# Optimization experiments

Measured on AMD Instinct MI355X. Metric: run time of the kernel, lower is better.

Reference implementation:

```python
import jax, jax.numpy as jnp
import numpy as np

TEMPERATURE = 0.5

def setup_inputs() -> dict:
    key = jax.random.key(0)
    k1, k2 = jax.random.split(key)
    B, D = 4096, 256
    return {
        "first_transformed": jax.random.normal(k1, (B, D), dtype=jnp.float32),
        "second_transformed": jax.random.normal(k2, (B, D), dtype=jnp.float32),
    }

def reference(first_transformed, second_transformed):
    B = first_transformed.shape[0]
    z = jnp.concatenate([first_transformed, second_transformed], axis=0)  # [2B, D]
    z = z / jnp.linalg.norm(z, axis=1, keepdims=True)
    sim = jnp.matmul(z, z.T) / TEMPERATURE  # [2B, 2B]
    n = 2 * B
    # exclude self-similarity from the denominator (mask diagonal)
    diag_mask = jnp.eye(n, dtype=bool)
    denom = jax.nn.logsumexp(jnp.where(diag_mask, -jnp.inf, sim), axis=1)  # [2B]
    # positive pair for row i is row (i+B) mod 2B
    pos_idx = (jnp.arange(n) + B) % n
    pos = sim[jnp.arange(n), pos_idx]  # [2B]
    # loss = 1/(2B) * sum_i (-log(exp(pos_i)/denom_i)) = mean(denom - pos)
    return jnp.mean(denom - pos)
```

## Files before the change

kernel.cpp:

```cpp
#include <hip/hip_runtime.h>
#include <hip/hip_bf16.h>
#include <math.h>


#define NROWS 8192
#define BHALF 4096
#define DDIM  256
#define ROWB  512
#define JSPLIT 8
#define JCHUNK (NROWS / JSPLIT)
#define JT 64
#define NTILES (JCHUNK / JT)
#define TILEB (JT * ROWB)

#define SQRT_K1 1.6986436f
#define LN2F 0.6931471805599453f

typedef __attribute__((ext_vector_type(8))) __bf16 bf16x8;
typedef __attribute__((ext_vector_type(4))) float f32x4;

#if __has_builtin(__builtin_amdgcn_exp2f)
#define FEXP2(x) __builtin_amdgcn_exp2f(x)
#else
#define FEXP2(x) __exp2f(x)
#endif
#if __has_builtin(__builtin_amdgcn_logf)
#define FLOG2(x) __builtin_amdgcn_logf(x)
#else
#define FLOG2(x) __log2f(x)
#endif

__device__ __forceinline__ float bfu(unsigned short u) {
  union { unsigned v; float f; } x; x.v = ((unsigned)u) << 16; return x.f;
}

__global__ __launch_bounds__(256) void norm_kernel(
    const float* __restrict__ a, const float* __restrict__ b,
    char* __restrict__ zb, float* __restrict__ selfdot) {
  int row = blockIdx.x * 4 + (threadIdx.x >> 6);
  int lane = threadIdx.x & 63;
  const float* src = (row < BHALF) ? (a + (size_t)row * DDIM)
                                   : (b + (size_t)(row - BHALF) * DDIM);
  float4 v = ((const float4*)src)[lane];
  float ss = v.x * v.x + v.y * v.y + v.z * v.z + v.w * v.w;
  #pragma unroll
  for (int m = 1; m < 64; m <<= 1) ss += __shfl_xor(ss, m, 64);
  float inv = rsqrtf(ss);
  inv = inv * (1.5f - 0.5f * ss * inv * inv);
  float sc = inv * SQRT_K1;

  union { __hip_bfloat16 h; unsigned short u; } c0, c1, c2, c3;
  c0.h = __float2bfloat16(v.x * sc);
  c1.h = __float2bfloat16(v.y * sc);
  c2.h = __float2bfloat16(v.z * sc);
  c3.h = __float2bfloat16(v.w * sc);
  float q0 = bfu(c0.u), q1 = bfu(c1.u), q2 = bfu(c2.u), q3 = bfu(c3.u);
  float sq = q0 * q0 + q1 * q1 + q2 * q2 + q3 * q3;
  #pragma unroll
  for (int m = 1; m < 64; m <<= 1) sq += __shfl_xor(sq, m, 64);

  ushort4 o = make_ushort4(c0.u, c1.u, c2.u, c3.u);
  int off = row * ROWB + ((lane * 8) ^ ((row & 7) << 4));
  *(ushort4*)(zb + off) = o;
  if (lane == 0) selfdot[row] = sq;
}

__global__ __launch_bounds__(512, 2) void sim_kernel(
    const char* __restrict__ zb, float* __restrict__ s_part) {
  __shared__ __align__(16) char lds[3 * TILEB];
  int js = blockIdx.x;
  int rb = blockIdx.y;
  int wave = threadIdx.x >> 6;
  int lane = threadIdx.x & 63;
  int lrow = lane & 15;
  int kgrp = lane >> 4;
  int sw = (lrow & 7) << 4;
  int r0 = rb * 256 + wave * 32;
  int jbase = js * JCHUNK;

  int koff[8];
  #pragma unroll
  for (int kk = 0; kk < 8; ++kk) koff[kk] = (kk * 64 + kgrp * 16) ^ sw;

  bf16x8 af[2][8];
  #pragma unroll
  for (int rf = 0; rf < 2; ++rf) {
    const char* rp = zb + (size_t)(r0 + rf * 16 + lrow) * ROWB;
    #pragma unroll
    for (int kk = 0; kk < 8; ++kk)
      af[rf][kk] = *(const bf16x8*)(rp + koff[kk]);
  }

  float sacc[2][4] = {};
  f32x4 X0, X1, Y0, Y1;
  X0 = X1 = Y0 = Y1 = (f32x4){-1e30f, -1e30f, -1e30f, -1e30f};

  #define STAGE1(dstbuf, j0, portion) do {                                    \
    const char* g_ = zb + (size_t)(j0) * ROWB + (portion) * 8192 +            \
                     wave * 1024 + lane * 16;                                 \
    char* l_ = lds + (dstbuf) * TILEB + (portion) * 8192 + wave * 1024;       \
    __builtin_amdgcn_global_load_lds(                                         \
        (const __attribute__((address_space(1))) void*)g_,                    \
        (__attribute__((address_space(3))) void*)l_, 16, 0, 0);               \
  } while (0)

  #define PHASE(ct, C0, C1, P0, P1) do {                                      \
    const char* lbr = lds + buf * TILEB + (ct) * 8192 + lrow * ROWB;          \
    bf16x8 bfv[8];                                                            \
    _Pragma("unroll")                                                         \
    for (int kk = 0; kk < 8; ++kk)                                            \
      bfv[kk] = *(const bf16x8*)(lbr + koff[kk]);                             \
    if (t + 2 < NTILES) STAGE1(dst, jbase + (t + 2) * JT, ct);                \
    _Pragma("unroll")                                                         \
    for (int r = 0; r < 4; ++r) {                                             \
      sacc[0][r] += FEXP2(P0[r]);                                             \
      sacc[1][r] += FEXP2(P1[r]);                                             \
    }                                                                         \
    __builtin_amdgcn_sched_barrier(0);                                        \
    __builtin_amdgcn_s_barrier();                                             \
    C0 = (f32x4){0.f, 0.f, 0.f, 0.f};                                         \
    C1 = (f32x4){0.f, 0.f, 0.f, 0.f};                                         \
    __builtin_amdgcn_s_setprio(1);                                            \
    _Pragma("unroll")                                                         \
    for (int kk = 0; kk < 8; ++kk) {                                          \
      C0 = __builtin_amdgcn_mfma_f32_16x16x32_bf16(af[0][kk], bfv[kk], C0, 0, 0, 0); \
      C1 = __builtin_amdgcn_mfma_f32_16x16x32_bf16(af[1][kk], bfv[kk], C1, 0, 0, 0); \
    }                                                                         \
    __builtin_amdgcn_s_setprio(0);                                            \
    if ((ct) == 3) {                                                          \
      if (t + 2 < NTILES)                                                     \
        asm volatile("s_waitcnt vmcnt(4)" ::: "memory");                      \
      else if (t + 1 < NTILES)                                                \
        asm volatile("s_waitcnt vmcnt(0)" ::: "memory");                      \
      __builtin_amdgcn_sched_barrier(0);                                      \
    }                                                                         \
    __builtin_amdgcn_s_barrier();                                             \
  } while (0)

  #pragma unroll
  for (int p = 0; p < 4; ++p) STAGE1(0, jbase, p);
  #pragma unroll
  for (int p = 0; p < 4; ++p) STAGE1(1, jbase + JT, p);
  asm volatile("s_waitcnt vmcnt(4)" ::: "memory");
  __builtin_amdgcn_sched_barrier(0);
  __builtin_amdgcn_s_barrier();

  int buf = 0;
  for (int t = 0; t < NTILES; ++t) {
    int dst = buf + 2; if (dst >= 3) dst -= 3;
    PHASE(0, X0, X1, Y0, Y1);
    PHASE(1, Y0, Y1, X0, X1);
    PHASE(2, X0, X1, Y0, Y1);
    PHASE(3, Y0, Y1, X0, X1);
    ++buf; if (buf == 3) buf = 0;
  }
  #pragma unroll
  for (int r = 0; r < 4; ++r) {
    sacc[0][r] += FEXP2(Y0[r]);
    sacc[1][r] += FEXP2(Y1[r]);
  }
  #undef PHASE
  #undef STAGE1

  #pragma unroll
  for (int rf = 0; rf < 2; ++rf) {
    #pragma unroll
    for (int r = 0; r < 4; ++r) {
      float v = sacc[rf][r];
      #pragma unroll
      for (int m = 1; m < 16; m <<= 1) v += __shfl_xor(v, m, 64);
      if (lrow == 0) {
        int grow = r0 + rf * 16 + kgrp * 4 + r;
        s_part[(size_t)grow * JSPLIT + js] = v;
      }
    }
  }
}

__global__ __launch_bounds__(256) void rowterm_kernel(
    const char* __restrict__ zb, const float* __restrict__ s_part,
    const float* __restrict__ selfdot, float* __restrict__ bpart) {
  int wave = threadIdx.x >> 6;
  int lane = threadIdx.x & 63;
  int rbase = blockIdx.x * 16 + wave * 4;
  float wacc = 0.f;
  #pragma unroll
  for (int rr = 0; rr < 4; ++rr) {
    int i = rbase + rr;
    int j = i ^ BHALF;
    int wo = (lane * 8) ^ ((i & 7) << 4);
    ushort4 zi = *(const ushort4*)(zb + (size_t)i * ROWB + wo);
    ushort4 zj = *(const ushort4*)(zb + (size_t)j * ROWB + wo);
    float dot = bfu(zi.x) * bfu(zj.x) + bfu(zi.y) * bfu(zj.y) +
                bfu(zi.z) * bfu(zj.z) + bfu(zi.w) * bfu(zj.w);
    float sp = (lane < JSPLIT) ? s_part[(size_t)i * JSPLIT + lane] : 0.f;
    #pragma unroll
    for (int m = 1; m < 64; m <<= 1) {
      dot += __shfl_xor(dot, m, 64);
      sp += __shfl_xor(sp, m, 64);
    }
    float S = sp - FEXP2(selfdot[i]);
    wacc += LN2F * (FLOG2(S) - dot);
  }
  __shared__ float red[4];
  if (lane == 0) red[wave] = wacc;
  __syncthreads();
  if (threadIdx.x == 0)
    bpart[blockIdx.x] = red[0] + red[1] + red[2] + red[3];
}

__global__ __launch_bounds__(512) void final_kernel(
    const float* __restrict__ bpart, float* __restrict__ out) {
  int t = threadIdx.x;
  float v = bpart[t];
  #pragma unroll
  for (int m = 1; m < 64; m <<= 1) v += __shfl_xor(v, m, 64);
  __shared__ float r2[8];
  if ((t & 63) == 0) r2[t >> 6] = v;
  __syncthreads();
  if (t == 0) {
    float s = 0.f;
    #pragma unroll
    for (int w = 0; w < 8; ++w) s += r2[w];
    out[0] = s / (float)NROWS;
  }
}

extern "C" void kernel_launch(void* const* d_in, const int* in_sizes, int n_in,
                              void* d_out, int out_size, void* d_ws, size_t ws_size,
                              hipStream_t stream) {
  const float* a = (const float*)d_in[0];
  const float* b = (const float*)d_in[1];
  float* out = (float*)d_out;
  char* ws = (char*)d_ws;

  char* zb = ws;
  float* selfdot = (float*)(ws + (size_t)NROWS * ROWB);
  float* s_part = selfdot + NROWS;
  float* bpart = s_part + (size_t)NROWS * JSPLIT;

  hipLaunchKernelGGL(norm_kernel, dim3(NROWS / 4), dim3(256), 0, stream,
                     a, b, zb, selfdot);
  hipLaunchKernelGGL(sim_kernel, dim3(JSPLIT, 32), dim3(512), 0, stream,
                     zb, s_part);
  hipLaunchKernelGGL(rowterm_kernel, dim3(512), dim3(256), 0, stream,
                     zb, s_part, selfdot, bpart);
  hipLaunchKernelGGL(final_kernel, dim3(1), dim3(512), 0, stream, bpart, out);
}
```

Measured before the change: 49.96 us.

## Exploit symmetry of similarity matrix by computing only upper-triangle tiles

Replaces the full row-by-column-chunk sweep with a tiled GEMM over 256x128 block pairs that covers only about half of the symmetric similarity matrix, using 1088 blocks. Each tile contributes exp-sums to both its rows and its columns, written into a wider per-row slot array that the rowterm kernel then sums. The inner loop moves from a resident-A, streamed-B scheme to K-sliced double-buffered staging of both operands with large register accumulators. This aims to roughly halve MFMA and exp work, at the cost of extra LDS reductions, more partial slots and higher register pressure.

```diff
diff --git a/kernel.cpp b/kernel.cpp
--- a/kernel.cpp
+++ b/kernel.cpp
@@ -7,11 +7,10 @@
 #define BHALF 4096
 #define DDIM  256
 #define ROWB  512
-#define JSPLIT 8
-#define JCHUNK (NROWS / JSPLIT)
-#define JT 64
-#define NTILES (JCHUNK / JT)
-#define TILEB (JT * ROWB)
+#define NKS   8
+#define BUFB  (24 * 1024)
+#define SSTRIDE 64
+#define NSLOT 49
 
 #define SQRT_K1 1.6986436f
 #define LN2F 0.6931471805599453f
@@ -65,114 +64,128 @@
   if (lane == 0) selfdot[row] = sq;
 }
 
-__global__ __launch_bounds__(512, 2) void sim_kernel(
+__global__ __launch_bounds__(256, 2) void sim_kernel(
     const char* __restrict__ zb, float* __restrict__ s_part) {
-  __shared__ __align__(16) char lds[3 * TILEB];
-  int js = blockIdx.x;
-  int rb = blockIdx.y;
+  __shared__ __align__(16) char lds[2 * BUFB];
+  __shared__ float cred_row[2][256];
+  __shared__ float cred_col[2][128];
+
+  int bid = blockIdx.x;
+  int h = bid & 1;
+  int tg = bid >> 1;
+  int t = tg & 31;
+  int g = tg >> 5;
+  int u = (t + g) & 31;
+  int r0 = t * 256;
+  int c0 = u * 256 + h * 128;
+
   int wave = threadIdx.x >> 6;
+  int wm = wave >> 1, wn = wave & 1;
   int lane = threadIdx.x & 63;
   int lrow = lane & 15;
   int kgrp = lane >> 4;
   int sw = (lrow & 7) << 4;
-  int r0 = rb * 256 + wave * 32;
-  int jbase = js * JCHUNK;
-
-  int koff[8];
-  #pragma unroll
-  for (int kk = 0; kk < 8; ++kk) koff[kk] = (kk * 64 + kgrp * 16) ^ sw;
-
-  bf16x8 af[2][8];
-  #pragma unroll
-  for (int rf = 0; rf < 2; ++rf) {
-    const char* rp = zb + (size_t)(r0 + rf * 16 + lrow) * ROWB;
-    #pragma unroll
-    for (int kk = 0; kk < 8; ++kk)
-      af[rf][kk] = *(const bf16x8*)(rp + koff[kk]);
-  }
-
-  float sacc[2][4] = {};
-  f32x4 X0, X1, Y0, Y1;
-  X0 = X1 = Y0 = Y1 = (f32x4){-1e30f, -1e30f, -1e30f, -1e30f};
-
-  #define STAGE1(dstbuf, j0, portion) do {                                    \
-    const char* g_ = zb + (size_t)(j0) * ROWB + (portion) * 8192 +            \
-                     wave * 1024 + lane * 16;                                 \
-    char* l_ = lds + (dstbuf) * TILEB + (portion) * 8192 + wave * 1024;       \
+
+  f32x4 acc[8][4];
+  #pragma unroll
+  for (int mi = 0; mi < 8; ++mi)
+    #pragma unroll
+    for (int nj = 0; nj < 4; ++nj)
+      acc[mi][nj] = (f32x4){0.f, 0.f, 0.f, 0.f};
+  bf16x8 bfv[4];
+
+  #define STAGE_SLOT(dstbuf, ks, s) do {                                      \
+    int rowb_ = ((s) < 16) ? (r0 + (s) * 16) : (c0 + ((s) - 16) * 16);        \
+    const char* g_ = zb + (size_t)(rowb_ + lrow) * ROWB +                     \
+                     (((ks) * 64 + kgrp * 16) ^ sw);                          \
+    char* l_ = lds + (dstbuf) * BUFB + (s) * 1024;                            \
     __builtin_amdgcn_global_load_lds(                                         \
         (const __attribute__((address_space(1))) void*)g_,                    \
         (__attribute__((address_space(3))) void*)l_, 16, 0, 0);               \
   } while (0)
 
-  #define PHASE(ct, C0, C1, P0, P1) do {                                      \
-    const char* lbr = lds + buf * TILEB + (ct) * 8192 + lrow * ROWB;          \
-    bf16x8 bfv[8];                                                            \
+  #define PHASE(P) do {                                                       \
+    const char* lb_ = lds + buf * BUFB + lane * 16;                           \
+    bf16x8 afv[4];                                                            \
     _Pragma("unroll")                                                         \
-    for (int kk = 0; kk < 8; ++kk)                                            \
-      bfv[kk] = *(const bf16x8*)(lbr + koff[kk]);                             \
-    if (t + 2 < NTILES) STAGE1(dst, jbase + (t + 2) * JT, ct);                \
-    _Pragma("unroll")                                                         \
-    for (int r = 0; r < 4; ++r) {                                             \
-      sacc[0][r] += FEXP2(P0[r]);                                             \
-      sacc[1][r] += FEXP2(P1[r]);                                             \
+    for (int i = 0; i < 4; ++i)                                               \
+      afv[i] = *(const bf16x8*)(lb_ + (wm * 8 + (P) * 4 + i) * 1024);         \
+    if ((P) == 0) {                                                           \
+      _Pragma("unroll")                                                       \
+      for (int nj = 0; nj < 4; ++nj)                                          \
+        bfv[nj] = *(const bf16x8*)(lb_ + (16 + wn * 4 + nj) * 1024);          \
     }                                                                         \
+    if (ks + 1 < NKS) {                                                       \
+      STAGE_SLOT(buf ^ 1, ks + 1, wave + 4 * (3 * (P) + 0));                  \
+      STAGE_SLOT(buf ^ 1, ks + 1, wave + 4 * (3 * (P) + 1));                  \
+      STAGE_SLOT(buf ^ 1, ks + 1, wave + 4 * (3 * (P) + 2));                  \
+    }                                                                         \
+    asm volatile("s_waitcnt lgkmcnt(0)" ::: "memory");                        \
     __builtin_amdgcn_sched_barrier(0);                                        \
     __builtin_amdgcn_s_barrier();                                             \
-    C0 = (f32x4){0.f, 0.f, 0.f, 0.f};                                         \
-    C1 = (f32x4){0.f, 0.f, 0.f, 0.f};                                         \
     __builtin_amdgcn_s_setprio(1);                                            \
     _Pragma("unroll")                                                         \
-    for (int kk = 0; kk < 8; ++kk) {                                          \
-      C0 = __builtin_amdgcn_mfma_f32_16x16x32_bf16(af[0][kk], bfv[kk], C0, 0, 0, 0); \
-      C1 = __builtin_amdgcn_mfma_f32_16x16x32_bf16(af[1][kk], bfv[kk], C1, 0, 0, 0); \
-    }                                                                         \
+    for (int i = 0; i < 4; ++i)                                               \
+      _Pragma("unroll")                                                       \
+      for (int nj = 0; nj < 4; ++nj)                                          \
+        acc[(P) * 4 + i][nj] = __builtin_amdgcn_mfma_f32_16x16x32_bf16(       \
+            afv[i], bfv[nj], acc[(P) * 4 + i][nj], 0, 0, 0);                  \
     __builtin_amdgcn_s_setprio(0);                                            \
-    if ((ct) == 3) {                                                          \
-      if (t + 2 < NTILES)                                                     \
-        asm volatile("s_waitcnt vmcnt(4)" ::: "memory");                      \
-      else if (t + 1 < NTILES)                                                \
-        asm volatile("s_waitcnt vmcnt(0)" ::: "memory");                      \
-      __builtin_amdgcn_sched_barrier(0);                                      \
-    }                                                                         \
+    if ((P) == 1 && ks + 1 < NKS)                                             \
+      asm volatile("s_waitcnt vmcnt(0)" ::: "memory");                        \
+    __builtin_amdgcn_sched_barrier(0);                                        \
     __builtin_amdgcn_s_barrier();                                             \
   } while (0)
 
   #pragma unroll
-  for (int p = 0; p < 4; ++p) STAGE1(0, jbase, p);
-  #pragma unroll
-  for (int p = 0; p < 4; ++p) STAGE1(1, jbase + JT, p);
-  asm volatile("s_waitcnt vmcnt(4)" ::: "memory");
+  for (int i = 0; i < 6; ++i) STAGE_SLOT(0, 0, wave + 4 * i);
+  asm volatile("s_waitcnt vmcnt(0)" ::: "memory");
   __builtin_amdgcn_sched_barrier(0);
   __builtin_amdgcn_s_barrier();
 
-  int buf = 0;
-  for (int t = 0; t < NTILES; ++t) {
-    int dst = buf + 2; if (dst >= 3) dst -= 3;
-    PHASE(0, X0, X1, Y0, Y1);
-    PHASE(1, Y0, Y1, X0, X1);
-    PHASE(2, X0, X1, Y0, Y1);
-    PHASE(3, Y0, Y1, X0, X1);
-    ++buf; if (buf == 3) buf = 0;
-  }
-  #pragma unroll
-  for (int r = 0; r < 4; ++r) {
-    sacc[0][r] += FEXP2(Y0[r]);
-    sacc[1][r] += FEXP2(Y1[r]);
+  for (int ks = 0; ks < NKS; ++ks) {
+    int buf = ks & 1;
+    PHASE(0);
+    PHASE(1);
   }
   #undef PHASE
-  #undef STAGE1
-
-  #pragma unroll
-  for (int rf = 0; rf < 2; ++rf) {
+  #undef STAGE_SLOT
+
+  float colp[4] = {0.f, 0.f, 0.f, 0.f};
+  #pragma unroll
+  for (int mi = 0; mi < 8; ++mi) {
     #pragma unroll
     for (int r = 0; r < 4; ++r) {
-      float v = sacc[rf][r];
-      #pragma unroll
-      for (int m = 1; m < 16; m <<= 1) v += __shfl_xor(v, m, 64);
-      if (lrow == 0) {
-        int grow = r0 + rf * 16 + kgrp * 4 + r;
-        s_part[(size_t)grow * JSPLIT + js] = v;
-      }
+      float e0 = FEXP2(acc[mi][0][r]);
+      float e1 = FEXP2(acc[mi][1][r]);
+      float e2 = FEXP2(acc[mi][2][r]);
+      float e3 = FEXP2(acc[mi][3][r]);
+      colp[0] += e0; colp[1] += e1; colp[2] += e2; colp[3] += e3;
+      float rs = (e0 + e1) + (e2 + e3);
+      rs += __shfl_xor(rs, 1, 64);
+      rs += __shfl_xor(rs, 2, 64);
+      rs += __shfl_xor(rs, 4, 64);
+      rs += __shfl_xor(rs, 8, 64);
+      if (lrow == 0)
+        cred_row[wn][wm * 128 + mi * 16 + kgrp * 4 + r] = rs;
+    }
+  }
+  #pragma unroll
+  for (int nj = 0; nj < 4; ++nj) {
+    float v = colp[nj];
+    v += __shfl_xor(v, 16, 64);
+    v += __shfl_xor(v, 32, 64);
+    if (kgrp == 0) cred_col[wm][wn * 64 + nj * 16 + lrow] = v;
+  }
+  __syncthreads();
+
+  {
+    int i0 = threadIdx.x;
+    float v = cred_row[0][i0] + cred_row[1][i0];
+    s_part[(size_t)(r0 + i0) * SSTRIDE + (2 * g + h)] = v;
+    if (g >= 1 && g <= 15 && i0 < 128) {
+      float c = cred_col[0][i0] + cred_col[1][i0];
+      s_part[(size_t)(c0 + i0) * SSTRIDE + (33 + g)] = c;
     }
   }
 }
@@ -193,7 +206,7 @@
     ushort4 zj = *(const ushort4*)(zb + (size_t)j * ROWB + wo);
     float dot = bfu(zi.x) * bfu(zj.x) + bfu(zi.y) * bfu(zj.y) +
                 bfu(zi.z) * bfu(zj.z) + bfu(zi.w) * bfu(zj.w);
-    float sp = (lane < JSPLIT) ? s_part[(size_t)i * JSPLIT + lane] : 0.f;
+    float sp = (lane < NSLOT) ? s_part[(size_t)i * SSTRIDE + lane] : 0.f;
     #pragma unroll
     for (int m = 1; m < 64; m <<= 1) {
       dot += __shfl_xor(dot, m, 64);
@@ -237,11 +250,11 @@
   char* zb = ws;
   float* selfdot = (float*)(ws + (size_t)NROWS * ROWB);
   float* s_part = selfdot + NROWS;
-  float* bpart = s_part + (size_t)NROWS * JSPLIT;
+  float* bpart = s_part + (size_t)NROWS * SSTRIDE;
 
   hipLaunchKernelGGL(norm_kernel, dim3(NROWS / 4), dim3(256), 0, stream,
                      a, b, zb, selfdot);
-  hipLaunchKernelGGL(sim_kernel, dim3(JSPLIT, 32), dim3(512), 0, stream,
+  hipLaunchKernelGGL(sim_kernel, dim3(1088), dim3(256), 0, stream,
                      zb, s_part);
   hipLaunchKernelGGL(rowterm_kernel, dim3(512), dim3(256), 0, stream,
                      zb, s_part, selfdot, bpart);
```

Result: slower. 55.13 us (+10.3%).
